# Optimization experiments

Measured on AMD Instinct MI355X. Metric: run time of the kernel, lower is better.

Reference implementation:

```python
import jax, jax.numpy as jnp
import numpy as np

ALPHA = 0.9        # synaptic decay (hidden layers; layer 0 uses 0*syn + h)
BETA = 0.85        # membrane leak
THRESHOLD = 1.0
SIM_TIME = 50
SCALE = 100.0      # SurrGradSpike.scale


@jax.custom_vjp
def spike_fn(x):
    # Heaviside step: 1.0 where x > 0 (strict, matching torch `input > 0`)
    return (x > 0).astype(x.dtype)

def _spike_fwd(x):
    return spike_fn(x), x

def _spike_bwd(x, g):
    # normalized fast-sigmoid surrogate gradient (Zenke & Ganguli 2018)
    return (g / (SCALE * jnp.abs(x) + 1.0) ** 2,)

spike_fn.defvjp(_spike_fwd, _spike_bwd)


def setup_inputs() -> dict:
    key = jax.random.key(0)
    k0, k1, k2, k3 = jax.random.split(key, 4)
    return {
        "inputs": jax.random.normal(k0, (128, 1024), dtype=jnp.float32),
        "W0": jax.random.normal(k1, (1024, 2048), dtype=jnp.float32),
        "W1": jax.random.normal(k2, (2048, 2048), dtype=jnp.float32),
        "W2": jax.random.normal(k3, (2048, 512), dtype=jnp.float32),
    }


def _dsnn_forward(inputs, weights):
    batch = inputs.shape[0]
    n_layers = len(weights)
    syn0 = tuple(jnp.zeros((batch, W.shape[1]), dtype=inputs.dtype) for W in weights)
    mem0 = tuple(jnp.zeros((batch, W.shape[1]), dtype=inputs.dtype) for W in weights)

    def step(carry, _):
        syn, mem = carry
        new_syn, new_mem = [], []
        prev_spk = None
        for l, W in enumerate(weights):
            # feedforward drive: static input at layer 0, current-step spikes after
            h = inputs @ W if l == 0 else prev_spk @ W
            # layer 0: new_syn = 0*syn + h ; others: alpha*syn + h
            s = h if l == 0 else ALPHA * syn[l] + h
            m = BETA * mem[l] + s
            mthr = m - THRESHOLD
            out = spike_fn(mthr)
            if l < n_layers - 1:
                # hard reset to 0 where spiked (output layer never resets)
                m = jnp.where(mthr > 0, jnp.zeros_like(m), m)
            prev_spk = out
            new_syn.append(s)
            new_mem.append(m)
        return (tuple(new_syn), tuple(new_mem)), None

    (syn, mem), _ = jax.lax.scan(step, (syn0, mem0), None, length=SIM_TIME)
    # torch returns mem_rec[-1][-1]: output-layer membrane at final timestep
    return mem[-1]


def reference(inputs, W0, W1, W2):
    return _dsnn_forward(inputs, (W0, W1, W2))
```

## Files before the change

### kernel.cpp

```cpp
#include <hip/hip_runtime.h>
#include <hip/hip_bf16.h>

#define ALPHA 0.9f
#define BETA  0.85f
#define TSIM  50
#define BATCH 128
#define N0    1024
#define N1    2048
#define N2    2048
#define N3    512

#define A50   0.00515379f
#define B50   0.000295764f
#define INVAB 20.0f

typedef __attribute__((ext_vector_type(8))) short bf16x8;
typedef __attribute__((ext_vector_type(4))) float f32x4;

#define GLOBAL_AS __attribute__((address_space(1)))
#define LDS_AS    __attribute__((address_space(3)))

#define R25(X) X(0) X(1) X(2) X(3) X(4) X(5) X(6) X(7) X(8) X(9) X(10) X(11) \
               X(12) X(13) X(14) X(15) X(16) X(17) X(18) X(19) X(20) X(21)   \
               X(22) X(23) X(24)

#define DECLC(t) float c##t = 0.f;
#define PROBE(t) c##t += w * (float)((p >> (t)) & 1u);
#define STEPT(t)                                                  \
    s = ALPHA * s + (base + c##t);                                \
    m = BETA * m + s;                                             \
    if (m - 1.f > 0.f) { a2 += (pa - pb) * INVAB; m = 0.f; }      \
    pa *= inva;                                                   \
    pb *= invb;

__global__ __launch_bounds__(256) void gemm_f32_splitk(const float* __restrict__ A,
                                                       const float* __restrict__ B,
                                                       float* __restrict__ Cp,
                                                       int M, int N, int K, int KC) {
    __shared__ float As[16][65];
    __shared__ float Bs[16][68];

    const int tid = threadIdx.x;
    const int tx  = tid % 16;
    const int ty  = tid / 16;
    const int bx  = blockIdx.x;
    const int by  = blockIdx.y;
    const int z   = blockIdx.z;

    float acc[4][4] = {};

    const int ar = tid / 4;
    const int ak = (tid % 4) * 4;
    const int br = tid / 16;
    const int bc = (tid % 16) * 4;

    const int kbeg = z * KC;
    for (int k0 = kbeg; k0 < kbeg + KC; k0 += 16) {
        float4 av = *(const float4*)&A[(size_t)(by * 64 + ar) * K + k0 + ak];
        As[ak + 0][ar] = av.x;
        As[ak + 1][ar] = av.y;
        As[ak + 2][ar] = av.z;
        As[ak + 3][ar] = av.w;
        float4 bv = *(const float4*)&B[(size_t)(k0 + br) * N + bx * 64 + bc];
        *(float4*)&Bs[br][bc] = bv;
        __syncthreads();

#pragma unroll
        for (int kk = 0; kk < 16; ++kk) {
            float a0 = As[kk][ty * 4 + 0];
            float a1 = As[kk][ty * 4 + 1];
            float a2 = As[kk][ty * 4 + 2];
            float a3 = As[kk][ty * 4 + 3];
            float b0 = Bs[kk][tx * 4 + 0];
            float b1 = Bs[kk][tx * 4 + 1];
            float b2 = Bs[kk][tx * 4 + 2];
            float b3 = Bs[kk][tx * 4 + 3];
            acc[0][0] += a0 * b0; acc[0][1] += a0 * b1; acc[0][2] += a0 * b2; acc[0][3] += a0 * b3;
            acc[1][0] += a1 * b0; acc[1][1] += a1 * b1; acc[1][2] += a1 * b2; acc[1][3] += a1 * b3;
            acc[2][0] += a2 * b0; acc[2][1] += a2 * b1; acc[2][2] += a2 * b2; acc[2][3] += a2 * b3;
            acc[3][0] += a3 * b0; acc[3][1] += a3 * b1; acc[3][2] += a3 * b2; acc[3][3] += a3 * b3;
        }
        __syncthreads();
    }

#pragma unroll
    for (int i = 0; i < 4; ++i) {
        float4 v = make_float4(acc[i][0], acc[i][1], acc[i][2], acc[i][3]);
        *(float4*)&Cp[((size_t)z * M + by * 64 + ty * 4 + i) * N + bx * 64 + tx * 4] = v;
    }
}

__global__ __launch_bounds__(256) void split_transpose(const float* __restrict__ W,
                                                       __hip_bfloat16* __restrict__ Th,
                                                       __hip_bfloat16* __restrict__ Tl,
                                                       int K, int N) {
    __shared__ float tile[32][33];
    const int tx = threadIdx.x % 32;
    const int ty = threadIdx.x / 32;
    const int k0 = blockIdx.y * 32;
    const int n0 = blockIdx.x * 32;

#pragma unroll
    for (int i = 0; i < 4; ++i)
        tile[ty + i * 8][tx] = W[(size_t)(k0 + ty + i * 8) * N + n0 + tx];
    __syncthreads();

#pragma unroll
    for (int i = 0; i < 4; ++i) {
        const float w = tile[tx][ty + i * 8];
        const __hip_bfloat16 hi = __float2bfloat16(w);
        const float lo = w - __bfloat162float(hi);
        const size_t o = (size_t)(n0 + ty + i * 8) * K + k0 + tx;
        Th[o] = hi;
        Tl[o] = __float2bfloat16(lo);
    }
}

template <int BN, int WGM, int WGN, int WMT, int WNT>
__global__ __launch_bounds__(256) void gemm_bf16_split_k(const __hip_bfloat16* __restrict__ A,
                                                         const __hip_bfloat16* __restrict__ Bh,
                                                         const __hip_bfloat16* __restrict__ Bl,
                                                         float* __restrict__ Cp,
                                                         int M, int N, int K, int KC) {
    constexpr int BM = 128;
    constexpr int BK = 32;
    constexpr int NA = (BM * BK) / (256 * 8);
    constexpr int NB = (BN * BK) / (256 * 8);

    __shared__ alignas(16) __hip_bfloat16 As[BM * BK];
    __shared__ alignas(16) __hip_bfloat16 Bhs[BN * BK];
    __shared__ alignas(16) __hip_bfloat16 Bls[BN * BK];

    const int tid  = threadIdx.x;
    const int wave = tid >> 6;
    const int lane = tid & 63;
    const int quad = lane >> 4;
    const int l16  = lane & 15;

    const int m0 = blockIdx.y * BM;
    const int n0 = blockIdx.x * BN;
    const int z  = blockIdx.z;

    const int wm = (wave % WGM) * (WMT * 16);
    const int wn = (wave / WGM) * (WNT * 16);

    f32x4 acc[WMT][WNT] = {};

    const __hip_bfloat16* agp[NA];
    int aoff[NA];
#pragma unroll
    for (int i = 0; i < NA; ++i) {
        const int c = i * 256 + tid;
        agp[i]  = A + (size_t)(m0 + (c >> 2)) * K + (c & 3) * 8;
        aoff[i] = c * 8;
    }
    const __hip_bfloat16 *bhgp[NB], *blgp[NB];
    int boff[NB];
#pragma unroll
    for (int i = 0; i < NB; ++i) {
        const int c = i * 256 + tid;
        bhgp[i] = Bh + (size_t)(n0 + (c >> 2)) * K + (c & 3) * 8;
        blgp[i] = Bl + (size_t)(n0 + (c >> 2)) * K + (c & 3) * 8;
        boff[i] = c * 8;
    }

    const int kbeg = z * KC;
    for (int k0 = kbeg; k0 < kbeg + KC; k0 += BK) {
#pragma unroll
        for (int i = 0; i < NA; ++i)
            __builtin_amdgcn_global_load_lds((const GLOBAL_AS void*)(agp[i] + k0),
                                             (LDS_AS void*)&As[aoff[i]], 16, 0, 0);
#pragma unroll
        for (int i = 0; i < NB; ++i) {
            __builtin_amdgcn_global_load_lds((const GLOBAL_AS void*)(bhgp[i] + k0),
                                             (LDS_AS void*)&Bhs[boff[i]], 16, 0, 0);
            __builtin_amdgcn_global_load_lds((const GLOBAL_AS void*)(blgp[i] + k0),
                                             (LDS_AS void*)&Bls[boff[i]], 16, 0, 0);
        }
        __syncthreads();

        bf16x8 af[WMT], bhf[WNT], blf[WNT];
#pragma unroll
        for (int i = 0; i < WMT; ++i)
            af[i] = *(const bf16x8*)&As[(wm + i * 16 + l16) * BK + quad * 8];
#pragma unroll
        for (int j = 0; j < WNT; ++j) {
            bhf[j] = *(const bf16x8*)&Bhs[(wn + j * 16 + l16) * BK + quad * 8];
            blf[j] = *(const bf16x8*)&Bls[(wn + j * 16 + l16) * BK + quad * 8];
        }
#pragma unroll
        for (int i = 0; i < WMT; ++i)
#pragma unroll
            for (int j = 0; j < WNT; ++j) {
                acc[i][j] = __builtin_amdgcn_mfma_f32_16x16x32_bf16(af[i], bhf[j], acc[i][j], 0, 0, 0);
                acc[i][j] = __builtin_amdgcn_mfma_f32_16x16x32_bf16(af[i], blf[j], acc[i][j], 0, 0, 0);
            }
        __syncthreads();
    }

#pragma unroll
    for (int i = 0; i < WMT; ++i)
#pragma unroll
        for (int j = 0; j < WNT; ++j)
#pragma unroll
            for (int r = 0; r < 4; ++r)
                Cp[((size_t)z * M + m0 + wm + i * 16 + quad * 4 + r) * N + n0 + wn + j * 16 + l16] =
                    acc[i][j][r];
}

__global__ __launch_bounds__(256) void scan_l0_classify(const float* __restrict__ P0,
                                                        __hip_bfloat16* __restrict__ C0,
                                                        int* __restrict__ jlist0,
                                                        unsigned long long* __restrict__ mask0,
                                                        int* __restrict__ count0) {
    const int b     = blockIdx.x;
    const int chunk = blockIdx.y;
    const int tid   = threadIdx.x;
    const int j     = chunk * 256 + tid;
    const int lane  = tid & 63;
    const int wv    = tid >> 6;

    float h = 0.f;
#pragma unroll
    for (int z = 0; z < 8; ++z) h += P0[((size_t)z * BATCH + b) * N1 + j];

    float m = 0.f;
    unsigned long long mask = 0ull;
#pragma unroll
    for (int t = 0; t < TSIM; ++t) {
        m = BETA * m + h;
        if (m - 1.f > 0.f) { mask |= (1ull << t); m = 0.f; }
    }
    const unsigned long long FULL = (1ull << TSIM) - 1ull;
    C0[(size_t)b * N1 + j] = __float2bfloat16((mask == FULL) ? 1.f : 0.f);

    const bool has = (mask != 0ull) && (mask != FULL);
    const unsigned long long bal = __ballot(has);

    __shared__ int wcnt[4];
    if (lane == 0) wcnt[wv] = __popcll(bal);
    __syncthreads();
    int base = 0;
#pragma unroll
    for (int w = 0; w < 4; ++w)
        if (w < wv) base += wcnt[w];
    const int pos = base + __popcll(bal & ((1ull << lane) - 1ull));

    const size_t lbase = (size_t)(b * 8 + chunk) * 256;
    if (has) {
        jlist0[lbase + pos] = j;
        mask0[lbase + pos]  = mask;
    }
    if (tid == 0) count0[b * 8 + chunk] = wcnt[0] + wcnt[1] + wcnt[2] + wcnt[3];
}

__global__ __launch_bounds__(256, 4) void h1_scan_a2(const float* __restrict__ PB1,
                                                     const float* __restrict__ W1,
                                                     const int* __restrict__ jlist0,
                                                     const unsigned long long* __restrict__ mask0,
                                                     const int* __restrict__ count0,
                                                     float* __restrict__ A2) {
    const int b  = blockIdx.x;
    const int jc = blockIdx.y * 256 + threadIdx.x;

    float base = 0.f;
#pragma unroll
    for (int z = 0; z < 16; ++z) base += PB1[((size_t)z * BATCH + b) * N2 + jc];

    float s = 0.f, m = 0.f, a2 = 0.f;
    float pa = A50, pb = B50;
    const float inva = 1.0f / ALPHA, invb = 1.0f / BETA;

    {
        R25(DECLC)
        for (int c = 0; c < 8; ++c) {
            const int cnt      = count0[b * 8 + c];
            const size_t lbase = (size_t)(b * 8 + c) * 256;
            for (int e = 0; e < cnt; ++e) {
                const unsigned p = (unsigned)mask0[lbase + e] & 0x1FFFFFFu;
                const int j      = jlist0[lbase + e];
                const float w    = W1[(size_t)j * N2 + jc];
                R25(PROBE)
            }
        }
        R25(STEPT)
    }

    {
        R25(DECLC)
        for (int c = 0; c < 8; ++c) {
            const int cnt      = count0[b * 8 + c];
            const size_t lbase = (size_t)(b * 8 + c) * 256;
            for (int e = 0; e < cnt; ++e) {
                const unsigned p = (unsigned)(mask0[lbase + e] >> 25) & 0x1FFFFFFu;
                const int j      = jlist0[lbase + e];
                const float w    = W1[(size_t)j * N2 + jc];
                R25(PROBE)
            }
        }
        R25(STEPT)
    }

    A2[(size_t)b * N2 + jc] = a2;
}

__global__ __launch_bounds__(256) void reduce_out(const float* __restrict__ PB2,
                                                  float* __restrict__ out) {
    const int idx = blockIdx.x * 256 + threadIdx.x;
    float v = 0.f;
#pragma unroll
    for (int z = 0; z < 16; ++z) v += PB2[(size_t)z * (BATCH * N3) + idx];
    out[idx] = v;
}

extern "C" void kernel_launch(void* const* d_in, const int* in_sizes, int n_in,
                              void* d_out, int out_size, void* d_ws, size_t ws_size,
                              hipStream_t stream) {
    const float* inputs = (const float*)d_in[0];
    const float* W0     = (const float*)d_in[1];
    const float* W1     = (const float*)d_in[2];
    const float* W2     = (const float*)d_in[3];
    float* out = (float*)d_out;

    float* P0  = (float*)d_ws;
    float* PB1 = P0 + 8 * BATCH * N1;
    float* A2  = PB1 + 16 * BATCH * N2;
    float* PB2 = A2 + BATCH * N2;
    unsigned long long* mk0 = (unsigned long long*)(PB2 + 16 * BATCH * N3);
    __hip_bfloat16* C0bf = (__hip_bfloat16*)(mk0 + BATCH * 8 * 256);
    __hip_bfloat16* W1th = C0bf + (size_t)BATCH * N1;
    __hip_bfloat16* W1tl = W1th + (size_t)N2 * N1;
    int* jl0  = (int*)(W1tl + (size_t)N2 * N1);
    int* cnt0 = jl0 + BATCH * 8 * 256;

    split_transpose<<<dim3(N2 / 32, N1 / 32), 256, 0, stream>>>(W1, W1th, W1tl, N1, N2);

    gemm_f32_splitk<<<dim3(N1 / 64, BATCH / 64, 8), 256, 0, stream>>>(
        inputs, W0, P0, BATCH, N1, N0, N0 / 8);

    scan_l0_classify<<<dim3(BATCH, N1 / 256), 256, 0, stream>>>(P0, C0bf, jl0, mk0, cnt0);

    gemm_bf16_split_k<128, 2, 2, 4, 4>
        <<<dim3(N2 / 128, BATCH / 128, 16), 256, 0, stream>>>(
            C0bf, W1th, W1tl, PB1, BATCH, N2, N1, N1 / 16);

    h1_scan_a2<<<dim3(BATCH, N2 / 256), 256, 0, stream>>>(
        PB1, W1, jl0, mk0, cnt0, A2);

    gemm_f32_splitk<<<dim3(N3 / 64, BATCH / 64, 16), 256, 0, stream>>>(
        A2, W2, PB2, BATCH, N3, N2, N2 / 16);

    reduce_out<<<(BATCH * N3) / 256, 256, 0, stream>>>(PB2, out);
}
```

Before: 153.2 us.

## Fuse stage-0 kernels, stage spike lists in LDS, unroll probe loop, retune split-K

Merges the W1 split-transpose and the layer-0 fp32 GEMM into one launch, using block-index ranges to pick the work. The h1 scan kernel now copies the compacted spike index and mask lists into shared memory once per block, then processes four entries per iteration so more W1 gathers are in flight. The split-K factor drops from 16 to 8 for the bf16 GEMM (now with a 64-wide N tile) and for the final GEMM, which halves partial-sum traffic and reduction work. In exchange each split does more serial K work and has fewer blocks, and the h1 kernel uses 24 KB of LDS, which may limit occupancy.

```diff
diff --git a/kernel.cpp b/kernel.cpp
--- a/kernel.cpp
+++ b/kernel.cpp
@@ -25,7 +25,10 @@
                X(22) X(23) X(24)
 
 #define DECLC(t) float c##t = 0.f;
-#define PROBE(t) c##t += w * (float)((p >> (t)) & 1u);
+#define PROBE4(t) c##t += w0 * (float)((p0 >> (t)) & 1u); \
+                  c##t += w1 * (float)((p1 >> (t)) & 1u); \
+                  c##t += w2 * (float)((p2 >> (t)) & 1u); \
+                  c##t += w3 * (float)((p3 >> (t)) & 1u);
 #define STEPT(t)                                                  \
     s = ALPHA * s + (base + c##t);                                \
     m = BETA * m + s;                                             \
@@ -33,19 +36,15 @@
     pa *= inva;                                                   \
     pb *= invb;
 
-__global__ __launch_bounds__(256) void gemm_f32_splitk(const float* __restrict__ A,
-                                                       const float* __restrict__ B,
-                                                       float* __restrict__ Cp,
-                                                       int M, int N, int K, int KC) {
-    __shared__ float As[16][65];
-    __shared__ float Bs[16][68];
-
+__device__ __forceinline__ void gemm_f32_core(const float* __restrict__ A,
+                                              const float* __restrict__ B,
+                                              float* __restrict__ Cp,
+                                              int M, int N, int K, int KC,
+                                              int bx, int by, int z,
+                                              float As[16][65], float Bs[16][68]) {
     const int tid = threadIdx.x;
     const int tx  = tid % 16;
     const int ty  = tid / 16;
-    const int bx  = blockIdx.x;
-    const int by  = blockIdx.y;
-    const int z   = blockIdx.z;
 
     float acc[4][4] = {};
 
@@ -90,30 +89,53 @@
     }
 }
 
-__global__ __launch_bounds__(256) void split_transpose(const float* __restrict__ W,
-                                                       __hip_bfloat16* __restrict__ Th,
-                                                       __hip_bfloat16* __restrict__ Tl,
-                                                       int K, int N) {
+__global__ __launch_bounds__(256) void stage0_fused(const float* __restrict__ W1,
+                                                    __hip_bfloat16* __restrict__ Th,
+                                                    __hip_bfloat16* __restrict__ Tl,
+                                                    const float* __restrict__ inputs,
+                                                    const float* __restrict__ W0,
+                                                    float* __restrict__ P0) {
+    __shared__ float As[16][65];
+    __shared__ float Bs[16][68];
     __shared__ float tile[32][33];
-    const int tx = threadIdx.x % 32;
-    const int ty = threadIdx.x / 32;
-    const int k0 = blockIdx.y * 32;
-    const int n0 = blockIdx.x * 32;
-
-#pragma unroll
-    for (int i = 0; i < 4; ++i)
-        tile[ty + i * 8][tx] = W[(size_t)(k0 + ty + i * 8) * N + n0 + tx];
-    __syncthreads();
-
-#pragma unroll
-    for (int i = 0; i < 4; ++i) {
-        const float w = tile[tx][ty + i * 8];
-        const __hip_bfloat16 hi = __float2bfloat16(w);
-        const float lo = w - __bfloat162float(hi);
-        const size_t o = (size_t)(n0 + ty + i * 8) * K + k0 + tx;
-        Th[o] = hi;
-        Tl[o] = __float2bfloat16(lo);
-    }
+
+    const int bid = blockIdx.x;
+    if (bid < 4096) {
+        const int tx = threadIdx.x % 32;
+        const int ty = threadIdx.x / 32;
+        const int n0 = (bid & 63) * 32;
+        const int k0 = (bid >> 6) * 32;
+
+#pragma unroll
+        for (int i = 0; i < 4; ++i)
+            tile[ty + i * 8][tx] = W1[(size_t)(k0 + ty + i * 8) * N2 + n0 + tx];
+        __syncthreads();
+
+#pragma unroll
+        for (int i = 0; i < 4; ++i) {
+            const float w = tile[tx][ty + i * 8];
+            const __hip_bfloat16 hi = __float2bfloat16(w);
+            const float lo = w - __bfloat162float(hi);
+            const size_t o = (size_t)(n0 + ty + i * 8) * N1 + k0 + tx;
+            Th[o] = hi;
+            Tl[o] = __float2bfloat16(lo);
+        }
+    } else {
+        const int g  = bid - 4096;
+        const int bx = g & 31;
+        const int by = (g >> 5) & 1;
+        const int z  = g >> 6;
+        gemm_f32_core(inputs, W0, P0, BATCH, N1, N0, N0 / 8, bx, by, z, As, Bs);
+    }
+}
+
+__global__ __launch_bounds__(256) void gemm_f32_splitk(const float* __restrict__ A,
+                                                       const float* __restrict__ B,
+                                                       float* __restrict__ Cp,
+                                                       int M, int N, int K, int KC) {
+    __shared__ float As[16][65];
+    __shared__ float Bs[16][68];
+    gemm_f32_core(A, B, Cp, M, N, K, KC, blockIdx.x, blockIdx.y, blockIdx.z, As, Bs);
 }
 
 template <int BN, int WGM, int WGN, int WMT, int WNT>
@@ -260,12 +282,36 @@
                                                      const unsigned long long* __restrict__ mask0,
                                                      const int* __restrict__ count0,
                                                      float* __restrict__ A2) {
-    const int b  = blockIdx.x;
-    const int jc = blockIdx.y * 256 + threadIdx.x;
+    const int b   = blockIdx.x;
+    const int tid = threadIdx.x;
+    const int jc  = blockIdx.y * 256 + tid;
+
+    __shared__ int      sj[2048];
+    __shared__ unsigned sml[2048];
+    __shared__ unsigned smh[2048];
+
+    int off[9];
+    off[0] = 0;
+#pragma unroll
+    for (int c = 0; c < 8; ++c) off[c + 1] = off[c] + count0[b * 8 + c];
+    const int tot = off[8];
+
+#pragma unroll
+    for (int c = 0; c < 8; ++c) {
+        const int cnt = off[c + 1] - off[c];
+        if (tid < cnt) {
+            const size_t lbase = (size_t)(b * 8 + c) * 256;
+            const unsigned long long mk = mask0[lbase + tid];
+            sj[off[c] + tid]  = jlist0[lbase + tid];
+            sml[off[c] + tid] = (unsigned)mk & 0x1FFFFFFu;
+            smh[off[c] + tid] = (unsigned)(mk >> 25) & 0x1FFFFFFu;
+        }
+    }
+    __syncthreads();
 
     float base = 0.f;
 #pragma unroll
-    for (int z = 0; z < 16; ++z) base += PB1[((size_t)z * BATCH + b) * N2 + jc];
+    for (int z = 0; z < 8; ++z) base += PB1[((size_t)z * BATCH + b) * N2 + jc];
 
     float s = 0.f, m = 0.f, a2 = 0.f;
     float pa = A50, pb = B50;
@@ -273,30 +319,30 @@
 
     {
         R25(DECLC)
-        for (int c = 0; c < 8; ++c) {
-            const int cnt      = count0[b * 8 + c];
-            const size_t lbase = (size_t)(b * 8 + c) * 256;
-            for (int e = 0; e < cnt; ++e) {
-                const unsigned p = (unsigned)mask0[lbase + e] & 0x1FFFFFFu;
-                const int j      = jlist0[lbase + e];
-                const float w    = W1[(size_t)j * N2 + jc];
-                R25(PROBE)
-            }
+        for (int e = 0; e < tot; e += 4) {
+            float w0 = 0.f, w1 = 0.f, w2 = 0.f, w3 = 0.f;
+            unsigned p0 = 0u, p1 = 0u, p2 = 0u, p3 = 0u;
+            p0 = sml[e];
+            w0 = W1[(size_t)sj[e] * N2 + jc];
+            if (e + 1 < tot) { p1 = sml[e + 1]; w1 = W1[(size_t)sj[e + 1] * N2 + jc]; }
+            if (e + 2 < tot) { p2 = sml[e + 2]; w2 = W1[(size_t)sj[e + 2] * N2 + jc]; }
+            if (e + 3 < tot) { p3 = sml[e + 3]; w3 = W1[(size_t)sj[e + 3] * N2 + jc]; }
+            R25(PROBE4)
         }
         R25(STEPT)
     }
 
     {
         R25(DECLC)
-        for (int c = 0; c < 8; ++c) {
-            const int cnt      = count0[b * 8 + c];
-            const size_t lbase = (size_t)(b * 8 + c) * 256;
-            for (int e = 0; e < cnt; ++e) {
-                const unsigned p = (unsigned)(mask0[lbase + e] >> 25) & 0x1FFFFFFu;
-                const int j      = jlist0[lbase + e];
-                const float w    = W1[(size_t)j * N2 + jc];
-                R25(PROBE)
-            }
+        for (int e = 0; e < tot; e += 4) {
+            float w0 = 0.f, w1 = 0.f, w2 = 0.f, w3 = 0.f;
+            unsigned p0 = 0u, p1 = 0u, p2 = 0u, p3 = 0u;
+            p0 = smh[e];
+            w0 = W1[(size_t)sj[e] * N2 + jc];
+            if (e + 1 < tot) { p1 = smh[e + 1]; w1 = W1[(size_t)sj[e + 1] * N2 + jc]; }
+            if (e + 2 < tot) { p2 = smh[e + 2]; w2 = W1[(size_t)sj[e + 2] * N2 + jc]; }
+            if (e + 3 < tot) { p3 = smh[e + 3]; w3 = W1[(size_t)sj[e + 3] * N2 + jc]; }
+            R25(PROBE4)
         }
         R25(STEPT)
     }
@@ -309,7 +355,7 @@
     const int idx = blockIdx.x * 256 + threadIdx.x;
     float v = 0.f;
 #pragma unroll
-    for (int z = 0; z < 16; ++z) v += PB2[(size_t)z * (BATCH * N3) + idx];
+    for (int z = 0; z < 8; ++z) v += PB2[(size_t)z * (BATCH * N3) + idx];
     out[idx] = v;
 }
 
@@ -324,31 +370,28 @@
 
     float* P0  = (float*)d_ws;
     float* PB1 = P0 + 8 * BATCH * N1;
-    float* A2  = PB1 + 16 * BATCH * N2;
+    float* A2  = PB1 + 8 * BATCH * N2;
     float* PB2 = A2 + BATCH * N2;
-    unsigned long long* mk0 = (unsigned long long*)(PB2 + 16 * BATCH * N3);
+    unsigned long long* mk0 = (unsigned long long*)(PB2 + 8 * BATCH * N3);
     __hip_bfloat16* C0bf = (__hip_bfloat16*)(mk0 + BATCH * 8 * 256);
     __hip_bfloat16* W1th = C0bf + (size_t)BATCH * N1;
     __hip_bfloat16* W1tl = W1th + (size_t)N2 * N1;
     int* jl0  = (int*)(W1tl + (size_t)N2 * N1);
     int* cnt0 = jl0 + BATCH * 8 * 256;
 
-    split_transpose<<<dim3(N2 / 32, N1 / 32), 256, 0, stream>>>(W1, W1th, W1tl, N1, N2);
-
-    gemm_f32_splitk<<<dim3(N1 / 64, BATCH / 64, 8), 256, 0, stream>>>(
-        inputs, W0, P0, BATCH, N1, N0, N0 / 8);
+    stage0_fused<<<4096 + 512, 256, 0, stream>>>(W1, W1th, W1tl, inputs, W0, P0);
 
     scan_l0_classify<<<dim3(BATCH, N1 / 256), 256, 0, stream>>>(P0, C0bf, jl0, mk0, cnt0);
 
-    gemm_bf16_split_k<128, 2, 2, 4, 4>
-        <<<dim3(N2 / 128, BATCH / 128, 16), 256, 0, stream>>>(
-            C0bf, W1th, W1tl, PB1, BATCH, N2, N1, N1 / 16);
+    gemm_bf16_split_k<64, 4, 1, 2, 4>
+        <<<dim3(N2 / 64, BATCH / 128, 8), 256, 0, stream>>>(
+            C0bf, W1th, W1tl, PB1, BATCH, N2, N1, N1 / 8);
 
     h1_scan_a2<<<dim3(BATCH, N2 / 256), 256, 0, stream>>>(
         PB1, W1, jl0, mk0, cnt0, A2);
 
-    gemm_f32_splitk<<<dim3(N3 / 64, BATCH / 64, 16), 256, 0, stream>>>(
-        A2, W2, PB2, BATCH, N3, N2, N2 / 16);
+    gemm_f32_splitk<<<dim3(N3 / 64, BATCH / 64, 8), 256, 0, stream>>>(
+        A2, W2, PB2, BATCH, N3, N2, N2 / 8);
 
     reduce_out<<<(BATCH * N3) / 256, 256, 0, stream>>>(PB2, out);
 }
```

Measured after the change: 170.8 us. +11.5%, slower.
